# Performance work log

Hardware: AMD Instinct MI355X
Metric: run time of the kernel (lower is better)

## Reference

```python
import jax, jax.numpy as jnp
import numpy as np

HEADS = 16
DIM_HEAD = 64
SCALE = DIM_HEAD ** -0.5


def setup_inputs() -> dict:
    key = jax.random.key(0)
    ks = jax.random.split(key, 5)
    b, n, dim = 2, 2048, 1024
    inner = HEADS * DIM_HEAD  # 1024
    std = dim ** -0.5
    return {
        "x": jax.random.normal(ks[0], (b, n, dim), jnp.float32),
        "ln_gamma": jnp.ones((dim,), jnp.float32),
        "ln_beta": jnp.zeros((dim,), jnp.float32),
        "W_qk": jax.random.normal(ks[1], (dim, 2 * inner), jnp.float32) * std,
        "W_v": jax.random.normal(ks[2], (dim, inner), jnp.float32) * std,
        "W_out": jax.random.normal(ks[3], (inner, dim), jnp.float32) * std,
        "b_out": jnp.zeros((dim,), jnp.float32),
    }


def _layernorm(x, gamma, beta, eps=1e-5):
    mu = jnp.mean(x, axis=-1, keepdims=True)
    var = jnp.var(x, axis=-1, keepdims=True)
    return (x - mu) * jax.lax.rsqrt(var + eps) * gamma + beta


def reference(x, ln_gamma, ln_beta, W_qk, W_v, W_out, b_out):
    b, n, dim = x.shape
    h, d = HEADS, DIM_HEAD
    xn = _layernorm(x, ln_gamma, ln_beta)
    qk = xn @ W_qk                      # [b, n, 2*h*d]
    q, k = jnp.split(qk, 2, axis=-1)    # each [b, n, h*d]
    v = xn @ W_v                        # [b, n, h*d]
    # b n (h d) -> b h n d
    q = q.reshape(b, n, h, d).transpose(0, 2, 1, 3)
    k = k.reshape(b, n, h, d).transpose(0, 2, 1, 3)
    v = v.reshape(b, n, h, d).transpose(0, 2, 1, 3)
    dots = jnp.einsum('bhid,bhjd->bhij', q, k) * SCALE
    attn = jax.nn.softmax(dots, axis=-1)
    out = jnp.einsum('bhij,bhjd->bhid', attn, v)
    out = out.transpose(0, 2, 1, 3).reshape(b, n, h * d)
    return out @ W_out + b_out
```

## Files before the change

kernel.cpp:

```cpp
#include <hip/hip_runtime.h>

#define HEADS 16
#define DHEAD 64
#define BATCH 2
#define SEQ   2048
#define DIM   1024
#define ROWS  (BATCH*SEQ)
#define SCALE_LOG2E 0.180336880f

typedef short v8s __attribute__((ext_vector_type(8)));
typedef float v4f __attribute__((ext_vector_type(4)));

__device__ __forceinline__ float fast_exp2(float x) {
    return __builtin_amdgcn_exp2f(x);
}

__device__ __forceinline__ unsigned short f2bf(float f) {
    unsigned u = __float_as_uint(f);
    u += 0x7FFFu + ((u >> 16) & 1u);
    return (unsigned short)(u >> 16);
}

__device__ __forceinline__ float bf2f(unsigned short u) {
    return __uint_as_float(((unsigned)u) << 16);
}

__device__ __forceinline__ unsigned pk_bf2(float hi, float lo) {
    return __builtin_amdgcn_perm(__float_as_uint(hi), __float_as_uint(lo), 0x07060302u);
}

#define GLDS16(g, l) __builtin_amdgcn_global_load_lds( \
    (__attribute__((address_space(1))) void*)(g), \
    (__attribute__((address_space(3))) void*)(l), 16, 0, 0)

__global__ __launch_bounds__(256) void prep_kernel(const float* __restrict__ x,
                                                   const float* __restrict__ gamma,
                                                   const float* __restrict__ beta,
                                                   const float* __restrict__ Wqk,
                                                   const float* __restrict__ Wv,
                                                   const float* __restrict__ Wout,
                                                   unsigned short* __restrict__ xn,
                                                   unsigned short* __restrict__ Tqk,
                                                   unsigned short* __restrict__ Tv,
                                                   unsigned short* __restrict__ To) {
    __shared__ float tile[64][65];
    __shared__ float ss[4], ssq[4];
    int gid = blockIdx.x;
    int t = threadIdx.x;
    if (gid < ROWS) {
        const float* xr = x + (size_t)gid * DIM;
        float4 v = *(const float4*)(xr + t * 4);
        float s  = v.x + v.y + v.z + v.w;
        float sq = v.x * v.x + v.y * v.y + v.z * v.z + v.w * v.w;
#pragma unroll
        for (int off = 32; off > 0; off >>= 1) {
            s  += __shfl_down(s,  off, 64);
            sq += __shfl_down(sq, off, 64);
        }
        int wave = t >> 6, lane = t & 63;
        if (lane == 0) { ss[wave] = s; ssq[wave] = sq; }
        __syncthreads();
        float tot  = ss[0] + ss[1] + ss[2] + ss[3];
        float totq = ssq[0] + ssq[1] + ssq[2] + ssq[3];
        float mean = tot * (1.f / DIM);
        float var  = totq * (1.f / DIM) - mean * mean;
        float rstd = rsqrtf(var + 1e-5f);
        float4 g = *(const float4*)(gamma + t * 4);
        float4 bb = *(const float4*)(beta + t * 4);
        ushort4 o;
        o.x = f2bf((v.x - mean) * rstd * g.x + bb.x);
        o.y = f2bf((v.y - mean) * rstd * g.y + bb.y);
        o.z = f2bf((v.z - mean) * rstd * g.z + bb.z);
        o.w = f2bf((v.w - mean) * rstd * g.w + bb.w);
        *(ushort4*)(xn + (size_t)gid * DIM + t * 4) = o;
        return;
    }
    int g2 = gid - ROWS;
    const float* W; unsigned short* Wt; int Nw, n0, k0;
    if (g2 < 512)      { W = Wqk;  Wt = Tqk; Nw = 2048; n0 = (g2 & 31) * 64; k0 = (g2 >> 5) * 64; }
    else if (g2 < 768) { int g3 = g2 - 512; W = Wv;  Wt = Tv; Nw = 1024; n0 = (g3 & 15) * 64; k0 = (g3 >> 4) * 64; }
    else               { int g3 = g2 - 768; W = Wout; Wt = To; Nw = 1024; n0 = (g3 & 15) * 64; k0 = (g3 >> 4) * 64; }
#pragma unroll
    for (int l = 0; l < 4; ++l) {
        int kk = (t >> 4) + l * 16;
        int nn = (t & 15) * 4;
        float4 v = *(const float4*)(W + (size_t)(k0 + kk) * Nw + n0 + nn);
        tile[kk][nn + 0] = v.x; tile[kk][nn + 1] = v.y;
        tile[kk][nn + 2] = v.z; tile[kk][nn + 3] = v.w;
    }
    __syncthreads();
#pragma unroll
    for (int l = 0; l < 4; ++l) {
        int cid = t + l * 256;
        int nn = cid >> 4, kc = (cid & 15) * 4;
        ushort4 o;
        o.x = f2bf(tile[kc + 0][nn]);
        o.y = f2bf(tile[kc + 1][nn]);
        o.z = f2bf(tile[kc + 2][nn]);
        o.w = f2bf(tile[kc + 3][nn]);
        *(ushort4*)(Wt + (size_t)(n0 + nn) * DIM + k0 + kc) = o;
    }
}

template<int BN, bool SWAP>
__device__ __forceinline__ void mm_core3(const unsigned short* __restrict__ A,
                                         const unsigned short* __restrict__ Bt,
                                         int K, int aTile, int bTile,
                                         unsigned short* As,
                                         unsigned short* Bs,
                                         v4f (*acc)[4]) {
    constexpr int MI = (BN == 128) ? 4 : 2;
    constexpr int BSLOT = (BN == 128) ? 4 : 2;
    int t = threadIdx.x;
    int w = t >> 6, L = t & 63, l15 = L & 15, quad = L >> 4;
    int aOffT = (BN == 128) ? (w >> 1) * 4 : w * 2;
    int bOffT = 0;
    if (BN == 128) bOffT = (w & 1) * 4;
    for (int k0 = 0; k0 < K; k0 += 64) {
        __syncthreads();
#pragma unroll
        for (int j = 0; j < 4; ++j) {
            int slot = w * 4 + j;
            int g = slot >> 1, kk = slot & 1;
            GLDS16(A + (size_t)(aTile + g * 16 + l15) * K + k0 + kk * 32 + quad * 8,
                   As + slot * 512);
        }
#pragma unroll
        for (int j = 0; j < BSLOT; ++j) {
            int slot = w * BSLOT + j;
            int g = slot >> 1, kk = slot & 1;
            GLDS16(Bt + (size_t)(bTile + g * 16 + l15) * K + k0 + kk * 32 + quad * 8,
                   Bs + slot * 512);
        }
        __syncthreads();
#pragma unroll
        for (int kk = 0; kk < 2; ++kk) {
            v8s a[MI], b[4];
#pragma unroll
            for (int i = 0; i < MI; ++i)
                a[i] = *(const v8s*)(As + ((aOffT + i) * 2 + kk) * 512 + L * 8);
#pragma unroll
            for (int j = 0; j < 4; ++j)
                b[j] = *(const v8s*)(Bs + ((bOffT + j) * 2 + kk) * 512 + L * 8);
#pragma unroll
            for (int i = 0; i < MI; ++i)
#pragma unroll
                for (int j = 0; j < 4; ++j)
                    acc[i][j] = SWAP
                        ? __builtin_amdgcn_mfma_f32_16x16x32_bf16(b[j], a[i], acc[i][j], 0, 0, 0)
                        : __builtin_amdgcn_mfma_f32_16x16x32_bf16(a[i], b[j], acc[i][j], 0, 0, 0);
        }
    }
}

__global__ __launch_bounds__(256) void gemm_qkv_kernel(const unsigned short* __restrict__ A,
                                                       const unsigned short* __restrict__ Bt,
                                                       unsigned short* __restrict__ q_h,
                                                       unsigned short* __restrict__ k_h,
                                                       unsigned short* __restrict__ v_t) {
    __shared__ __align__(16) unsigned short As[16 * 512];
    __shared__ __align__(16) unsigned short Bs[16 * 512];
    int t = threadIdx.x, w = t >> 6, L = t & 63, l15 = L & 15, quad = L >> 4;
    int aTile = blockIdx.y * 128, bTile = blockIdx.x * 128;
    int aOff = (w >> 1) * 64, bOff = (w & 1) * 64;
    v4f acc[4][4] = {};
    if (bTile < 2048) {
        mm_core3<128, true>(A, Bt, DIM, aTile, bTile, As, Bs, acc);
#pragma unroll
        for (int j = 0; j < 4; ++j) {
            int col = bTile + bOff + j * 16 + quad * 4;
            unsigned short* dst = (col < 1024) ? q_h : k_h;
            int c = col & 1023;
            int h = c >> 6, d = c & 63;
#pragma unroll
            for (int i = 0; i < 4; ++i) {
                int m = aTile + aOff + i * 16 + l15;
                int b = m >> 11, seq = m & 2047;
                ushort4 o;
                o.x = f2bf(acc[i][j][0]); o.y = f2bf(acc[i][j][1]);
                o.z = f2bf(acc[i][j][2]); o.w = f2bf(acc[i][j][3]);
                *(ushort4*)(dst + (((size_t)(b * 16 + h)) * SEQ + seq) * 64 + d) = o;
            }
        }
    } else {
        mm_core3<128, false>(A, Bt, DIM, aTile, bTile, As, Bs, acc);
#pragma unroll
        for (int j = 0; j < 4; ++j) {
            int c = bTile + bOff + j * 16 + l15 - 2048;
            int h = c >> 6, d = c & 63;
#pragma unroll
            for (int i = 0; i < 4; ++i) {
                int m0 = aTile + aOff + i * 16 + quad * 4;
                int b = m0 >> 11, seq0 = m0 & 2047;
                ushort4 o;
                o.x = f2bf(acc[i][j][0]); o.y = f2bf(acc[i][j][1]);
                o.z = f2bf(acc[i][j][2]); o.w = f2bf(acc[i][j][3]);
                *(ushort4*)(v_t + (((size_t)(b * 16 + h)) * 64 + d) * SEQ + seq0) = o;
            }
        }
    }
}

__global__ __launch_bounds__(256) void gemm_out_kernel(const unsigned short* __restrict__ A,
                                                       const unsigned short* __restrict__ Bt,
                                                       const float* __restrict__ bias,
                                                       float* __restrict__ C) {
    __shared__ __align__(16) unsigned short As[16 * 512];
    __shared__ __align__(16) unsigned short Bs[8 * 512];
    int t = threadIdx.x, w = t >> 6, L = t & 63, l15 = L & 15, quad = L >> 4;
    int aTile = blockIdx.y * 128, bTile = blockIdx.x * 64;
    v4f acc[2][4] = {};
    mm_core3<64, true>(A, Bt, DIM, aTile, bTile, As, Bs, acc);
#pragma unroll
    for (int j = 0; j < 4; ++j) {
        int n = bTile + j * 16 + quad * 4;
        float4 bv = *(const float4*)(bias + n);
#pragma unroll
        for (int i = 0; i < 2; ++i) {
            int m = aTile + w * 32 + i * 16 + l15;
            float4 o = make_float4(acc[i][j][0] + bv.x, acc[i][j][1] + bv.y,
                                   acc[i][j][2] + bv.z, acc[i][j][3] + bv.w);
            *(float4*)(C + (size_t)m * DIM + n) = o;
        }
    }
}

__global__ __launch_bounds__(256) void attn_kernel(const unsigned short* __restrict__ q_h,
                                                   const unsigned short* __restrict__ k_h,
                                                   const unsigned short* __restrict__ v_t,
                                                   unsigned short* __restrict__ opart,
                                                   float* __restrict__ lpart) {
    __shared__ __align__(16) unsigned short KF[8 * 64 * 8];
    __shared__ __align__(16) unsigned short VF[8 * 64 * 8];
    __shared__ __align__(16) unsigned short Pld[4][2][16 * 72];
    int qt = blockIdx.x >> 1, kh = blockIdx.x & 1;
    int h = blockIdx.y, b = blockIdx.z;
    int bh = b * HEADS + h;
    int w = threadIdx.x >> 6;
    int L = threadIdx.x & 63, l15 = L & 15, quad = L >> 4;

    const unsigned short* qp = q_h + ((size_t)bh * SEQ + qt * 128 + w * 32 + l15) * 64 + quad * 8;
    v8s qf[2][2];
    qf[0][0] = *(const v8s*)(qp);
    qf[0][1] = *(const v8s*)(qp + 32);
    qf[1][0] = *(const v8s*)(qp + 16 * 64);
    qf[1][1] = *(const v8s*)(qp + 16 * 64 + 32);

    const unsigned short* kstage = k_h + ((size_t)bh * SEQ + w * 16 + l15) * 64 + quad * 8;
    const unsigned short* vstage = v_t + ((size_t)bh * 64 + w * 16 + l15) * SEQ + quad * 8;

    v4f o[2][4] = {};
    v4f lacc[2] = {};
    const short ob = (short)0x3F80;
    const v8s ones = {ob, ob, ob, ob, ob, ob, ob, ob};

    int jbase = kh * 1024;
    v8s ks0 = *(const v8s*)(kstage + (size_t)jbase * 64);
    v8s ks1 = *(const v8s*)(kstage + (size_t)jbase * 64 + 32);
    v8s vs0 = *(const v8s*)(vstage + jbase);
    v8s vs1 = *(const v8s*)(vstage + jbase + 32);

    for (int jj = 0; jj < 1024; jj += 64) {
        int j0 = jbase + jj;
        __syncthreads();
        *(v8s*)&KF[((w * 2 + 0) * 64 + L) * 8] = ks0;
        *(v8s*)&KF[((w * 2 + 1) * 64 + L) * 8] = ks1;
        *(v8s*)&VF[((w * 2 + 0) * 64 + L) * 8] = vs0;
        *(v8s*)&VF[((w * 2 + 1) * 64 + L) * 8] = vs1;
        __syncthreads();
        if (jj + 64 < 1024) {
            ks0 = *(const v8s*)(kstage + (size_t)(j0 + 64) * 64);
            ks1 = *(const v8s*)(kstage + (size_t)(j0 + 64) * 64 + 32);
            vs0 = *(const v8s*)(vstage + j0 + 64);
            vs1 = *(const v8s*)(vstage + j0 + 64 + 32);
        }
        v8s kf[4][2], vf[4][2];
#pragma unroll
        for (int jt = 0; jt < 4; ++jt) {
            kf[jt][0] = *(const v8s*)&KF[((jt * 2 + 0) * 64 + L) * 8];
            kf[jt][1] = *(const v8s*)&KF[((jt * 2 + 1) * 64 + L) * 8];
            vf[jt][0] = *(const v8s*)&VF[((jt * 2 + 0) * 64 + L) * 8];
            vf[jt][1] = *(const v8s*)&VF[((jt * 2 + 1) * 64 + L) * 8];
        }
        v4f s[2][4] = {};
#pragma unroll
        for (int m = 0; m < 2; ++m)
#pragma unroll
            for (int jt = 0; jt < 4; ++jt) {
                s[m][jt] = __builtin_amdgcn_mfma_f32_16x16x32_bf16(kf[jt][0], qf[m][0], s[m][jt], 0, 0, 0);
                s[m][jt] = __builtin_amdgcn_mfma_f32_16x16x32_bf16(kf[jt][1], qf[m][1], s[m][jt], 0, 0, 0);
            }
#pragma unroll
        for (int m = 0; m < 2; ++m)
#pragma unroll
            for (int jt = 0; jt < 4; ++jt) {
                float p0 = fast_exp2(s[m][jt][0] * SCALE_LOG2E);
                float p1 = fast_exp2(s[m][jt][1] * SCALE_LOG2E);
                float p2 = fast_exp2(s[m][jt][2] * SCALE_LOG2E);
                float p3 = fast_exp2(s[m][jt][3] * SCALE_LOG2E);
                uint2 pk;
                pk.x = pk_bf2(p1, p0);
                pk.y = pk_bf2(p3, p2);
                *(uint2*)&Pld[w][m][l15 * 72 + jt * 16 + quad * 4] = pk;
            }
#pragma unroll
        for (int m = 0; m < 2; ++m) {
            v8s pb0 = *(const v8s*)&Pld[w][m][l15 * 72 + quad * 8];
            v8s pb1 = *(const v8s*)&Pld[w][m][l15 * 72 + 32 + quad * 8];
#pragma unroll
            for (int dt = 0; dt < 4; ++dt) {
                o[m][dt] = __builtin_amdgcn_mfma_f32_16x16x32_bf16(vf[dt][0], pb0, o[m][dt], 0, 0, 0);
                o[m][dt] = __builtin_amdgcn_mfma_f32_16x16x32_bf16(vf[dt][1], pb1, o[m][dt], 0, 0, 0);
            }
            lacc[m] = __builtin_amdgcn_mfma_f32_16x16x32_bf16(ones, pb0, lacc[m], 0, 0, 0);
            lacc[m] = __builtin_amdgcn_mfma_f32_16x16x32_bf16(ones, pb1, lacc[m], 0, 0, 0);
        }
    }
#pragma unroll
    for (int m = 0; m < 2; ++m) {
        int seq = qt * 128 + w * 32 + m * 16 + l15;
        int rowg = b * SEQ + seq;
        if (quad == 0)
            lpart[((size_t)(kh * 32 + bh)) * SEQ + seq] = lacc[m][0];
#pragma unroll
        for (int dt = 0; dt < 4; ++dt) {
            uint2 ov;
            ov.x = pk_bf2(o[m][dt][1], o[m][dt][0]);
            ov.y = pk_bf2(o[m][dt][3], o[m][dt][2]);
            *(uint2*)(opart + ((size_t)kh * ROWS + rowg) * DIM + h * 64 + dt * 16 + quad * 4) = ov;
        }
    }
}

__global__ __launch_bounds__(256) void combine_kernel(const unsigned short* __restrict__ opart,
                                                      const float* __restrict__ lpart,
                                                      unsigned short* __restrict__ ao) {
    int rowg = blockIdx.x, t = threadIdx.x;
    int b = rowg >> 11, seq = rowg & 2047;
    int h = t >> 4;
    int bh = b * 16 + h;
    float l0 = lpart[(size_t)bh * SEQ + seq];
    float l1 = lpart[((size_t)(32 + bh)) * SEQ + seq];
    float inv = 1.f / (l0 + l1);
    size_t base = (size_t)rowg * DIM + t * 4;
    ushort4 a0 = *(const ushort4*)(opart + base);
    ushort4 a1 = *(const ushort4*)(opart + (size_t)ROWS * DIM + base);
    ushort4 o;
    o.x = f2bf((bf2f(a0.x) + bf2f(a1.x)) * inv);
    o.y = f2bf((bf2f(a0.y) + bf2f(a1.y)) * inv);
    o.z = f2bf((bf2f(a0.z) + bf2f(a1.z)) * inv);
    o.w = f2bf((bf2f(a0.w) + bf2f(a1.w)) * inv);
    *(ushort4*)(ao + base) = o;
}

extern "C" void kernel_launch(void* const* d_in, const int* in_sizes, int n_in,
                              void* d_out, int out_size, void* d_ws, size_t ws_size,
                              hipStream_t stream) {
    const float* x     = (const float*)d_in[0];
    const float* gamma = (const float*)d_in[1];
    const float* beta  = (const float*)d_in[2];
    const float* Wqk   = (const float*)d_in[3];
    const float* Wv    = (const float*)d_in[4];
    const float* Wout  = (const float*)d_in[5];
    const float* bout  = (const float*)d_in[6];
    float* out = (float*)d_out;

    unsigned short* ws = (unsigned short*)d_ws;
    unsigned short* xn    = ws;
    unsigned short* Wt_qk = xn + (size_t)ROWS * DIM;
    unsigned short* Wt_v  = Wt_qk + (size_t)2048 * DIM;
    unsigned short* Wt_o  = Wt_v + (size_t)DIM * DIM;
    unsigned short* q_h   = Wt_o + (size_t)DIM * DIM;
    unsigned short* k_h   = q_h + (size_t)ROWS * DIM;
    unsigned short* v_t   = k_h + (size_t)ROWS * DIM;
    unsigned short* ao    = v_t + (size_t)ROWS * DIM;
    unsigned short* opart = ao + (size_t)ROWS * DIM;
    float*          lpart = (float*)(opart + (size_t)2 * ROWS * DIM);

    prep_kernel<<<ROWS + 1024, 256, 0, stream>>>(x, gamma, beta, Wqk, Wv, Wout,
                                                 xn, Wt_qk, Wt_v, Wt_o);
    gemm_qkv_kernel<<<dim3(3072 / 128, ROWS / 128), 256, 0, stream>>>(xn, Wt_qk, q_h, k_h, v_t);
    attn_kernel<<<dim3(2 * SEQ / 128, HEADS, BATCH), 256, 0, stream>>>(q_h, k_h, v_t, opart, lpart);
    combine_kernel<<<ROWS, 256, 0, stream>>>(opart, lpart, ao);
    gemm_out_kernel<<<dim3(DIM / 64, ROWS / 128), 256, 0, stream>>>(ao, Wt_o, bout, out);
}
```

Baseline: 230.0 us.

## Shrink GEMM K-step to 32, stage QKV epilogue through LDS, split prep kernel

The shared GEMM core now loads a 32-wide K slice per iteration instead of 64. This halves LDS tile size but doubles the number of barriers and loop trips. The QKV GEMM epilogue packs bf16 results into a padded LDS tile, then writes 16-byte coalesced rows to q/k and the transposed v layout, replacing scattered 8-byte stores. The fused prep kernel is split into a layernorm kernel and a 3D-grid weight transpose kernel, which adds one launch and leaves some idle blocks for the smaller matrices.

```diff
diff --git a/kernel.cpp b/kernel.cpp
--- a/kernel.cpp
+++ b/kernel.cpp
@@ -33,57 +33,58 @@
     (__attribute__((address_space(1))) void*)(g), \
     (__attribute__((address_space(3))) void*)(l), 16, 0, 0)
 
-__global__ __launch_bounds__(256) void prep_kernel(const float* __restrict__ x,
-                                                   const float* __restrict__ gamma,
-                                                   const float* __restrict__ beta,
-                                                   const float* __restrict__ Wqk,
-                                                   const float* __restrict__ Wv,
-                                                   const float* __restrict__ Wout,
-                                                   unsigned short* __restrict__ xn,
-                                                   unsigned short* __restrict__ Tqk,
-                                                   unsigned short* __restrict__ Tv,
-                                                   unsigned short* __restrict__ To) {
+__global__ __launch_bounds__(256) void ln_kernel(const float* __restrict__ x,
+                                                 const float* __restrict__ gamma,
+                                                 const float* __restrict__ beta,
+                                                 unsigned short* __restrict__ xn) {
+    int row = blockIdx.x;
+    const float* xr = x + (size_t)row * DIM;
+    int t = threadIdx.x;
+    float4 v = *(const float4*)(xr + t * 4);
+    float s  = v.x + v.y + v.z + v.w;
+    float sq = v.x * v.x + v.y * v.y + v.z * v.z + v.w * v.w;
+#pragma unroll
+    for (int off = 32; off > 0; off >>= 1) {
+        s  += __shfl_down(s,  off, 64);
+        sq += __shfl_down(sq, off, 64);
+    }
+    __shared__ float ss[4], ssq[4];
+    int wave = t >> 6, lane = t & 63;
+    if (lane == 0) { ss[wave] = s; ssq[wave] = sq; }
+    __syncthreads();
+    float tot  = ss[0] + ss[1] + ss[2] + ss[3];
+    float totq = ssq[0] + ssq[1] + ssq[2] + ssq[3];
+    float mean = tot * (1.f / DIM);
+    float var  = totq * (1.f / DIM) - mean * mean;
+    float rstd = rsqrtf(var + 1e-5f);
+    float4 g = *(const float4*)(gamma + t * 4);
+    float4 bb = *(const float4*)(beta + t * 4);
+    ushort4 o;
+    o.x = f2bf((v.x - mean) * rstd * g.x + bb.x);
+    o.y = f2bf((v.y - mean) * rstd * g.y + bb.y);
+    o.z = f2bf((v.z - mean) * rstd * g.z + bb.z);
+    o.w = f2bf((v.w - mean) * rstd * g.w + bb.w);
+    *(ushort4*)(xn + (size_t)row * DIM + t * 4) = o;
+}
+
+__global__ __launch_bounds__(256) void tr_all_kernel(const float* __restrict__ Wqk,
+                                                     const float* __restrict__ Wv,
+                                                     const float* __restrict__ Wout,
+                                                     unsigned short* __restrict__ Tqk,
+                                                     unsigned short* __restrict__ Tv,
+                                                     unsigned short* __restrict__ To) {
+    int z = blockIdx.z;
+    const float* W = (z == 0) ? Wqk : (z == 1) ? Wv : Wout;
+    unsigned short* Wt = (z == 0) ? Tqk : (z == 1) ? Tv : To;
+    int Nw = (z == 0) ? 2048 : 1024;
+    int n0 = blockIdx.x * 64, k0 = blockIdx.y * 64;
+    if (n0 >= Nw) return;
     __shared__ float tile[64][65];
-    __shared__ float ss[4], ssq[4];
-    int gid = blockIdx.x;
-    int t = threadIdx.x;
-    if (gid < ROWS) {
-        const float* xr = x + (size_t)gid * DIM;
-        float4 v = *(const float4*)(xr + t * 4);
-        float s  = v.x + v.y + v.z + v.w;
-        float sq = v.x * v.x + v.y * v.y + v.z * v.z + v.w * v.w;
-#pragma unroll
-        for (int off = 32; off > 0; off >>= 1) {
-            s  += __shfl_down(s,  off, 64);
-            sq += __shfl_down(sq, off, 64);
-        }
-        int wave = t >> 6, lane = t & 63;
-        if (lane == 0) { ss[wave] = s; ssq[wave] = sq; }
-        __syncthreads();
-        float tot  = ss[0] + ss[1] + ss[2] + ss[3];
-        float totq = ssq[0] + ssq[1] + ssq[2] + ssq[3];
-        float mean = tot * (1.f / DIM);
-        float var  = totq * (1.f / DIM) - mean * mean;
-        float rstd = rsqrtf(var + 1e-5f);
-        float4 g = *(const float4*)(gamma + t * 4);
-        float4 bb = *(const float4*)(beta + t * 4);
-        ushort4 o;
-        o.x = f2bf((v.x - mean) * rstd * g.x + bb.x);
-        o.y = f2bf((v.y - mean) * rstd * g.y + bb.y);
-        o.z = f2bf((v.z - mean) * rstd * g.z + bb.z);
-        o.w = f2bf((v.w - mean) * rstd * g.w + bb.w);
-        *(ushort4*)(xn + (size_t)gid * DIM + t * 4) = o;
-        return;
-    }
-    int g2 = gid - ROWS;
-    const float* W; unsigned short* Wt; int Nw, n0, k0;
-    if (g2 < 512)      { W = Wqk;  Wt = Tqk; Nw = 2048; n0 = (g2 & 31) * 64; k0 = (g2 >> 5) * 64; }
-    else if (g2 < 768) { int g3 = g2 - 512; W = Wv;  Wt = Tv; Nw = 1024; n0 = (g3 & 15) * 64; k0 = (g3 >> 4) * 64; }
-    else               { int g3 = g2 - 768; W = Wout; Wt = To; Nw = 1024; n0 = (g3 & 15) * 64; k0 = (g3 >> 4) * 64; }
+    int tid = threadIdx.x;
 #pragma unroll
     for (int l = 0; l < 4; ++l) {
-        int kk = (t >> 4) + l * 16;
-        int nn = (t & 15) * 4;
+        int kk = (tid >> 4) + l * 16;
+        int nn = (tid & 15) * 4;
         float4 v = *(const float4*)(W + (size_t)(k0 + kk) * Nw + n0 + nn);
         tile[kk][nn + 0] = v.x; tile[kk][nn + 1] = v.y;
         tile[kk][nn + 2] = v.z; tile[kk][nn + 3] = v.w;
@@ -91,7 +92,7 @@
     __syncthreads();
 #pragma unroll
     for (int l = 0; l < 4; ++l) {
-        int cid = t + l * 256;
+        int cid = tid + l * 256;
         int nn = cid >> 4, kc = (cid & 15) * 4;
         ushort4 o;
         o.x = f2bf(tile[kc + 0][nn]);
@@ -103,53 +104,49 @@
 }
 
 template<int BN, bool SWAP>
-__device__ __forceinline__ void mm_core3(const unsigned short* __restrict__ A,
+__device__ __forceinline__ void mm_core4(const unsigned short* __restrict__ A,
                                          const unsigned short* __restrict__ Bt,
                                          int K, int aTile, int bTile,
                                          unsigned short* As,
                                          unsigned short* Bs,
                                          v4f (*acc)[4]) {
     constexpr int MI = (BN == 128) ? 4 : 2;
-    constexpr int BSLOT = (BN == 128) ? 4 : 2;
     int t = threadIdx.x;
     int w = t >> 6, L = t & 63, l15 = L & 15, quad = L >> 4;
-    int aOffT = (BN == 128) ? (w >> 1) * 4 : w * 2;
-    int bOffT = 0;
-    if (BN == 128) bOffT = (w & 1) * 4;
-    for (int k0 = 0; k0 < K; k0 += 64) {
-        __syncthreads();
-#pragma unroll
-        for (int j = 0; j < 4; ++j) {
-            int slot = w * 4 + j;
-            int g = slot >> 1, kk = slot & 1;
-            GLDS16(A + (size_t)(aTile + g * 16 + l15) * K + k0 + kk * 32 + quad * 8,
+    int aSlot0 = (BN == 128) ? (w >> 1) * 4 : w * 2;
+    int bSlot0 = (BN == 128) ? (w & 1) * 4 : 0;
+    for (int k0 = 0; k0 < K; k0 += 32) {
+        __syncthreads();
+#pragma unroll
+        for (int j = 0; j < 2; ++j) {
+            int slot = w * 2 + j;
+            GLDS16(A + (size_t)(aTile + slot * 16 + l15) * K + k0 + quad * 8,
                    As + slot * 512);
         }
-#pragma unroll
-        for (int j = 0; j < BSLOT; ++j) {
-            int slot = w * BSLOT + j;
-            int g = slot >> 1, kk = slot & 1;
-            GLDS16(Bt + (size_t)(bTile + g * 16 + l15) * K + k0 + kk * 32 + quad * 8,
-                   Bs + slot * 512);
-        }
-        __syncthreads();
-#pragma unroll
-        for (int kk = 0; kk < 2; ++kk) {
-            v8s a[MI], b[4];
-#pragma unroll
-            for (int i = 0; i < MI; ++i)
-                a[i] = *(const v8s*)(As + ((aOffT + i) * 2 + kk) * 512 + L * 8);
+        if (BN == 128) {
+#pragma unroll
+            for (int j = 0; j < 2; ++j) {
+                int slot = w * 2 + j;
+                GLDS16(Bt + (size_t)(bTile + slot * 16 + l15) * K + k0 + quad * 8,
+                       Bs + slot * 512);
+            }
+        } else {
+            GLDS16(Bt + (size_t)(bTile + w * 16 + l15) * K + k0 + quad * 8,
+                   Bs + w * 512);
+        }
+        __syncthreads();
+        v8s a[MI], b[4];
+#pragma unroll
+        for (int i = 0; i < MI; ++i) a[i] = *(const v8s*)(As + (aSlot0 + i) * 512 + L * 8);
+#pragma unroll
+        for (int j = 0; j < 4; ++j) b[j] = *(const v8s*)(Bs + (bSlot0 + j) * 512 + L * 8);
+#pragma unroll
+        for (int i = 0; i < MI; ++i)
 #pragma unroll
             for (int j = 0; j < 4; ++j)
-                b[j] = *(const v8s*)(Bs + ((bOffT + j) * 2 + kk) * 512 + L * 8);
-#pragma unroll
-            for (int i = 0; i < MI; ++i)
-#pragma unroll
-                for (int j = 0; j < 4; ++j)
-                    acc[i][j] = SWAP
-                        ? __builtin_amdgcn_mfma_f32_16x16x32_bf16(b[j], a[i], acc[i][j], 0, 0, 0)
-                        : __builtin_amdgcn_mfma_f32_16x16x32_bf16(a[i], b[j], acc[i][j], 0, 0, 0);
-        }
+                acc[i][j] = SWAP
+                    ? __builtin_amdgcn_mfma_f32_16x16x32_bf16(b[j], a[i], acc[i][j], 0, 0, 0)
+                    : __builtin_amdgcn_mfma_f32_16x16x32_bf16(a[i], b[j], acc[i][j], 0, 0, 0);
     }
 }
 
@@ -158,45 +155,60 @@
                                                        unsigned short* __restrict__ q_h,
                                                        unsigned short* __restrict__ k_h,
                                                        unsigned short* __restrict__ v_t) {
-    __shared__ __align__(16) unsigned short As[16 * 512];
-    __shared__ __align__(16) unsigned short Bs[16 * 512];
+    __shared__ __align__(16) unsigned short buf[4 * 64 * 72];
+    unsigned short* As = buf;
+    unsigned short* Bs = buf + 4096;
     int t = threadIdx.x, w = t >> 6, L = t & 63, l15 = L & 15, quad = L >> 4;
     int aTile = blockIdx.y * 128, bTile = blockIdx.x * 128;
     int aOff = (w >> 1) * 64, bOff = (w & 1) * 64;
+    unsigned short* ct = buf + w * 4608;
     v4f acc[4][4] = {};
     if (bTile < 2048) {
-        mm_core3<128, true>(A, Bt, DIM, aTile, bTile, As, Bs, acc);
-#pragma unroll
-        for (int j = 0; j < 4; ++j) {
-            int col = bTile + bOff + j * 16 + quad * 4;
-            unsigned short* dst = (col < 1024) ? q_h : k_h;
-            int c = col & 1023;
-            int h = c >> 6, d = c & 63;
-#pragma unroll
-            for (int i = 0; i < 4; ++i) {
-                int m = aTile + aOff + i * 16 + l15;
-                int b = m >> 11, seq = m & 2047;
-                ushort4 o;
-                o.x = f2bf(acc[i][j][0]); o.y = f2bf(acc[i][j][1]);
-                o.z = f2bf(acc[i][j][2]); o.w = f2bf(acc[i][j][3]);
-                *(ushort4*)(dst + (((size_t)(b * 16 + h)) * SEQ + seq) * 64 + d) = o;
-            }
+        mm_core4<128, true>(A, Bt, DIM, aTile, bTile, As, Bs, acc);
+        __syncthreads();
+#pragma unroll
+        for (int i = 0; i < 4; ++i)
+#pragma unroll
+            for (int j = 0; j < 4; ++j) {
+                uint2 pk;
+                pk.x = pk_bf2(acc[i][j][1], acc[i][j][0]);
+                pk.y = pk_bf2(acc[i][j][3], acc[i][j][2]);
+                *(uint2*)&ct[(i * 16 + l15) * 72 + j * 16 + quad * 4] = pk;
+            }
+        int c0 = bTile + bOff;
+        unsigned short* dst = (c0 < 1024) ? q_h : k_h;
+        int h = (c0 & 1023) >> 6;
+        int m0 = aTile + aOff;
+        int b = m0 >> 11, seq0 = m0 & 2047;
+        unsigned short* base = dst + (((size_t)(b * 16 + h)) * SEQ + seq0) * 64;
+#pragma unroll
+        for (int i2 = 0; i2 < 8; ++i2) {
+            int row = i2 * 8 + (L >> 3);
+            v8s vv = *(const v8s*)&ct[row * 72 + (L & 7) * 8];
+            *(v8s*)(base + (size_t)i2 * 512 + L * 8) = vv;
         }
     } else {
-        mm_core3<128, false>(A, Bt, DIM, aTile, bTile, As, Bs, acc);
-#pragma unroll
-        for (int j = 0; j < 4; ++j) {
-            int c = bTile + bOff + j * 16 + l15 - 2048;
-            int h = c >> 6, d = c & 63;
-#pragma unroll
-            for (int i = 0; i < 4; ++i) {
-                int m0 = aTile + aOff + i * 16 + quad * 4;
-                int b = m0 >> 11, seq0 = m0 & 2047;
-                ushort4 o;
-                o.x = f2bf(acc[i][j][0]); o.y = f2bf(acc[i][j][1]);
-                o.z = f2bf(acc[i][j][2]); o.w = f2bf(acc[i][j][3]);
-                *(ushort4*)(v_t + (((size_t)(b * 16 + h)) * 64 + d) * SEQ + seq0) = o;
-            }
+        mm_core4<128, false>(A, Bt, DIM, aTile, bTile, As, Bs, acc);
+        __syncthreads();
+#pragma unroll
+        for (int i = 0; i < 4; ++i)
+#pragma unroll
+            for (int j = 0; j < 4; ++j) {
+                uint2 pk;
+                pk.x = pk_bf2(acc[i][j][1], acc[i][j][0]);
+                pk.y = pk_bf2(acc[i][j][3], acc[i][j][2]);
+                *(uint2*)&ct[(j * 16 + l15) * 72 + i * 16 + quad * 4] = pk;
+            }
+        int c0 = bTile + bOff - 2048;
+        int h = c0 >> 6;
+        int m0 = aTile + aOff;
+        int b = m0 >> 11, seq0 = m0 & 2047;
+        unsigned short* base = v_t + (((size_t)(b * 16 + h)) * 64) * SEQ + seq0;
+#pragma unroll
+        for (int i2 = 0; i2 < 8; ++i2) {
+            int d = i2 * 8 + (L >> 3);
+            v8s vv = *(const v8s*)&ct[d * 72 + (L & 7) * 8];
+            *(v8s*)(base + (size_t)d * SEQ + (L & 7) * 8) = vv;
         }
     }
 }
@@ -205,12 +217,12 @@
                                                        const unsigned short* __restrict__ Bt,
                                                        const float* __restrict__ bias,
                                                        float* __restrict__ C) {
-    __shared__ __align__(16) unsigned short As[16 * 512];
-    __shared__ __align__(16) unsigned short Bs[8 * 512];
+    __shared__ __align__(16) unsigned short As[8 * 512];
+    __shared__ __align__(16) unsigned short Bs[4 * 512];
     int t = threadIdx.x, w = t >> 6, L = t & 63, l15 = L & 15, quad = L >> 4;
     int aTile = blockIdx.y * 128, bTile = blockIdx.x * 64;
     v4f acc[2][4] = {};
-    mm_core3<64, true>(A, Bt, DIM, aTile, bTile, As, Bs, acc);
+    mm_core4<64, true>(A, Bt, DIM, aTile, bTile, As, Bs, acc);
 #pragma unroll
     for (int j = 0; j < 4; ++j) {
         int n = bTile + j * 16 + quad * 4;
@@ -377,8 +389,8 @@
     unsigned short* opart = ao + (size_t)ROWS * DIM;
     float*          lpart = (float*)(opart + (size_t)2 * ROWS * DIM);
 
-    prep_kernel<<<ROWS + 1024, 256, 0, stream>>>(x, gamma, beta, Wqk, Wv, Wout,
-                                                 xn, Wt_qk, Wt_v, Wt_o);
+    ln_kernel<<<ROWS, 256, 0, stream>>>(x, gamma, beta, xn);
+    tr_all_kernel<<<dim3(32, 16, 3), 256, 0, stream>>>(Wqk, Wv, Wout, Wt_qk, Wt_v, Wt_o);
     gemm_qkv_kernel<<<dim3(3072 / 128, ROWS / 128), 256, 0, stream>>>(xn, Wt_qk, q_h, k_h, v_t);
     attn_kernel<<<dim3(2 * SEQ / 128, HEADS, BATCH), 256, 0, stream>>>(q_h, k_h, v_t, opart, lpart);
     combine_kernel<<<ROWS, 256, 0, stream>>>(opart, lpart, ao);
```

Result: faster. 219.5 us (-4.5%).
